# Optimization experiments

Measured on AMD Instinct MI355X. Metric: run time of the kernel, lower is better.

The kernel has to match this reference:

```python
import jax, jax.numpy as jnp
import numpy as np

TOKENS, DIM, DIM_OUT, R, ALPHA = 8192, 4096, 4096, 16, 32
SCALE = ALPHA / R  # 2.0


def setup_inputs() -> dict:
    key = jax.random.key(0)
    k1, k2, k3, k4, k5 = jax.random.split(key, 5)
    x = jax.random.normal(k1, (TOKENS, DIM), dtype=jnp.float32)
    A = jax.random.normal(k2, (DIM, R), dtype=jnp.float32)
    B = jax.random.normal(k3, (R, DIM_OUT), dtype=jnp.float32) * 0.02
    W = jax.random.normal(k4, (DIM_OUT, DIM), dtype=jnp.float32) * 0.02  # base Linear weight
    b = jax.random.normal(k5, (DIM_OUT,), dtype=jnp.float32)
    return {"x": x, "A": A, "B": B, "W": W, "b": b}


def reference(x, A, B, W, b):
    # LoRA path: x @ (A @ B) * scale, computed in the efficient low-rank order
    # (mathematically identical to materializing the full-rank weight).
    lora = ((x @ A) @ B) * SCALE              # [tokens, dim_out]
    base = x @ W.T + b                         # wrapped base Linear forward
    return lora + base
```

## Files before the change

### kernel.cpp

```cpp
#include <hip/hip_runtime.h>
#include <hip/hip_bf16.h>
#include <stdint.h>

#define TOKENS   8192
#define DIM      4096
#define DIM_OUT  4096
#define LORA_R   16
#define LORA_SCALE 2.0f

typedef __bf16 bf16_t;
typedef __attribute__((ext_vector_type(8))) __bf16 bfrag;
typedef __attribute__((ext_vector_type(4))) float f32x4;

__device__ __forceinline__ void gload_lds16(const bf16_t* gsrc, bf16_t* ldst) {
    __builtin_amdgcn_global_load_lds(
        (const __attribute__((address_space(1))) uint32_t*)(const void*)gsrc,
        (__attribute__((address_space(3))) uint32_t*)(void*)ldst,
        16, 0, 0);
}

__global__ void cast_x_kernel(const float* __restrict__ x, bf16_t* __restrict__ xb) {
    const int total = TOKENS * DIM / 8;
    for (int i = blockIdx.x * blockDim.x + threadIdx.x; i < total;
         i += gridDim.x * blockDim.x) {
        const float4* p = reinterpret_cast<const float4*>(x + (size_t)i * 8);
        float4 v0 = p[0], v1 = p[1];
        union { bf16_t o[8]; uint4 u; } pk;
        pk.o[0] = (bf16_t)v0.x; pk.o[1] = (bf16_t)v0.y;
        pk.o[2] = (bf16_t)v0.z; pk.o[3] = (bf16_t)v0.w;
        pk.o[4] = (bf16_t)v1.x; pk.o[5] = (bf16_t)v1.y;
        pk.o[6] = (bf16_t)v1.z; pk.o[7] = (bf16_t)v1.w;
        *reinterpret_cast<uint4*>(xb + (size_t)i * 8) = pk.u;
    }
}

__global__ void weff_kernel(const float* __restrict__ W, const float* __restrict__ A,
                            const float* __restrict__ B, bf16_t* __restrict__ Wt) {
    int idx = blockIdx.x * blockDim.x + threadIdx.x;
    int k0 = (idx & 511) << 3;
    int n0 = (idx >> 9) << 2;

    float bn[4][16];
#pragma unroll
    for (int r = 0; r < 16; ++r) {
        float4 bv = *reinterpret_cast<const float4*>(B + (size_t)r * DIM_OUT + n0);
        bn[0][r] = bv.x; bn[1][r] = bv.y; bn[2][r] = bv.z; bn[3][r] = bv.w;
    }
    float ab[4][8];
#pragma unroll
    for (int j = 0; j < 8; ++j) {
        const float4* ap = reinterpret_cast<const float4*>(A + (size_t)(k0 + j) * LORA_R);
        float4 a0 = ap[0], a1 = ap[1], a2 = ap[2], a3 = ap[3];
        float av[16] = {a0.x,a0.y,a0.z,a0.w,a1.x,a1.y,a1.z,a1.w,
                        a2.x,a2.y,a2.z,a2.w,a3.x,a3.y,a3.z,a3.w};
#pragma unroll
        for (int n = 0; n < 4; ++n) {
            float s = 0.f;
#pragma unroll
            for (int r = 0; r < 16; ++r) s += av[r] * bn[n][r];
            ab[n][j] = s;
        }
    }
#pragma unroll
    for (int n = 0; n < 4; ++n) {
        const float4* wp = reinterpret_cast<const float4*>(W + (size_t)(n0 + n) * DIM + k0);
        float4 w0 = wp[0], w1 = wp[1];
        float wv[8] = {w0.x,w0.y,w0.z,w0.w,w1.x,w1.y,w1.z,w1.w};
        union { bf16_t o[8]; uint4 u; } pk;
#pragma unroll
        for (int j = 0; j < 8; ++j) pk.o[j] = (bf16_t)(wv[j] + LORA_SCALE * ab[n][j]);
        *reinterpret_cast<uint4*>(Wt + (size_t)(n0 + n) * DIM + k0) = pk.u;
    }
}

#define BM 256
#define BN 256
#define BK 64
#define MB_BLKS (TOKENS / BM)
#define NB_BLKS (DIM_OUT / BN)
#define NT      (DIM / BK)

#define SB0() __builtin_amdgcn_sched_barrier(0)
#define BAR() do { SB0(); __builtin_amdgcn_s_barrier(); SB0(); } while (0)
#define LGKM0() do { asm volatile("s_waitcnt lgkmcnt(0)" ::: "memory"); SB0(); } while (0)
#define VMWAIT_(n) asm volatile("s_waitcnt vmcnt(" #n ")" ::: "memory")
#define VMWAIT(n) VMWAIT_(n)

__global__ __launch_bounds__(512, 2) void gemm_kernel(
    const bf16_t* __restrict__ Xb, const bf16_t* __restrict__ Wt,
    const float* __restrict__ bias, float* __restrict__ C)
{
    __shared__ __align__(16) bf16_t sA[2][BM][BK];
    __shared__ __align__(16) bf16_t sB[2][BN][BK];

    const int nwg = MB_BLKS * NB_BLKS;
    int bid = blockIdx.x;
    int swz = (bid & 7) * (nwg >> 3) + (bid >> 3);
    int bm = swz / NB_BLKS;
    int bn = swz % NB_BLKS;

    const int tid  = threadIdx.x;
    const int lane = tid & 63;
    const int wid  = tid >> 6;
    const int wr   = wid >> 2;
    const int wc   = wid & 3;

    const int srow = tid >> 3;
    const int scol = (tid & 7) * 8;
    const int koff = (((tid & 7) ^ ((tid >> 3) & 7)) * 8);
    const bf16_t* Ag = Xb + (size_t)(bm * BM + srow) * DIM + koff;
    const bf16_t* Bg = Wt + (size_t)(bn * BN + srow) * DIM + koff;

#define STAGE_A_H(dd, kt, h) do { \
    const bf16_t* s_ = Ag + (size_t)(kt) * BK + (size_t)((h) * 128) * DIM; \
    bf16_t* d_ = &sA[dd][(h) * 128 + srow][scol]; \
    gload_lds16(s_,                    d_); \
    gload_lds16(s_ + (size_t)64 * DIM, d_ + 64 * BK); \
} while (0)

#define STAGE_B_H(dd, kt, h) do { \
    const bf16_t* s_ = Bg + (size_t)(kt) * BK + (size_t)((h) * 128) * DIM; \
    bf16_t* d_ = &sB[dd][(h) * 128 + srow][scol]; \
    gload_lds16(s_,                    d_); \
    gload_lds16(s_ + (size_t)64 * DIM, d_ + 64 * BK); \
} while (0)

    const int q     = lane & 7;
    const int kslot = lane >> 4;
    const int r15   = lane & 15;
    const int cK0   = ((kslot    ) ^ q) * 8;
    const int cK1   = ((kslot + 4) ^ q) * 8;
    const int arow0 = wr * 128 + r15;
    const int brow0 = wc * 64  + r15;

    f32x4 acc[8][4] = {};
    bfrag a[4][2], bLo[2][2], bHi[2][2];

#define READ_A4(dst, dd, mb) do { \
    _Pragma("unroll") \
    for (int m_ = 0; m_ < 4; ++m_) { \
        dst[m_][0] = *reinterpret_cast<const bfrag*>(&sA[dd][arow0 + (mb + m_) * 16][cK0]); \
        dst[m_][1] = *reinterpret_cast<const bfrag*>(&sA[dd][arow0 + (mb + m_) * 16][cK1]); \
    } \
} while (0)

#define READ_B2(dst, dd, nb) do { \
    _Pragma("unroll") \
    for (int n_ = 0; n_ < 2; ++n_) { \
        dst[n_][0] = *reinterpret_cast<const bfrag*>(&sB[dd][brow0 + (nb + n_) * 16][cK0]); \
        dst[n_][1] = *reinterpret_cast<const bfrag*>(&sB[dd][brow0 + (nb + n_) * 16][cK1]); \
    } \
} while (0)

#define MFMA_Q(Af, Bf, mb, nb) do { \
    __builtin_amdgcn_s_setprio(1); \
    _Pragma("unroll") \
    for (int m_ = 0; m_ < 4; ++m_) \
    _Pragma("unroll") \
    for (int n_ = 0; n_ < 2; ++n_) \
    _Pragma("unroll") \
    for (int ks_ = 0; ks_ < 2; ++ks_) \
        acc[mb + m_][nb + n_] = __builtin_amdgcn_mfma_f32_16x16x32_bf16( \
            Af[m_][ks_], Bf[n_][ks_], acc[mb + m_][nb + n_], 0, 0, 0); \
    __builtin_amdgcn_s_setprio(0); \
} while (0)

#define TILE(d, kt, S1, S2, VM) do { \
     READ_A4(a, d, 0); READ_B2(bLo, d, 0); \
             BAR(); LGKM0(); MFMA_Q(a, bLo, 0, 0); BAR(); \
     READ_B2(bHi, d, 2); \
             if (S1) STAGE_A_H((d) ^ 1, (kt) + 1, 1); \
             BAR(); LGKM0(); MFMA_Q(a, bHi, 0, 2); BAR(); \
     READ_A4(a, d, 4); \
             if (S2) STAGE_B_H(d, (kt) + 2, 0); \
             BAR(); LGKM0(); MFMA_Q(a, bHi, 4, 2); BAR(); \
     if (S2) { STAGE_B_H(d, (kt) + 2, 1); STAGE_A_H(d, (kt) + 2, 0); } \
             BAR(); MFMA_Q(a, bLo, 4, 0); VMWAIT(VM); BAR(); \
} while (0)

    STAGE_A_H(0, 0, 0); STAGE_A_H(0, 0, 1); STAGE_B_H(0, 0, 0); STAGE_B_H(0, 0, 1);
    STAGE_A_H(1, 1, 0); STAGE_B_H(1, 1, 0); STAGE_B_H(1, 1, 1);
    VMWAIT(6);
    BAR();

    for (int it = 0; it < NT / 2 - 1; ++it) {
        int kt0 = 2 * it;
        TILE(0, kt0,     true, true, 6);
        TILE(1, kt0 + 1, true, true, 6);
    }
    TILE(0, 62, true,  false, 0);
    TILE(1, 63, false, false, 0);

    int row0 = bm * BM + wr * 128 + (lane >> 4) * 4;
    int col0 = bn * BN + wc * 64 + r15;
#pragma unroll
    for (int n = 0; n < 4; ++n) {
        int c = col0 + n * 16;
        float bv = bias[c];
#pragma unroll
        for (int m = 0; m < 8; ++m) {
            int r = row0 + m * 16;
#pragma unroll
            for (int j = 0; j < 4; ++j)
                C[(size_t)(r + j) * DIM_OUT + c] = acc[m][n][j] + bv;
        }
    }
}

extern "C" void kernel_launch(void* const* d_in, const int* in_sizes, int n_in,
                              void* d_out, int out_size, void* d_ws, size_t ws_size,
                              hipStream_t stream) {
    const float* x = (const float*)d_in[0];
    const float* A = (const float*)d_in[1];
    const float* B = (const float*)d_in[2];
    const float* W = (const float*)d_in[3];
    const float* b = (const float*)d_in[4];
    float* out = (float*)d_out;

    bf16_t* xb = (bf16_t*)d_ws;
    bf16_t* Wt = (bf16_t*)((char*)d_ws + (size_t)TOKENS * DIM * 2);

    cast_x_kernel<<<2048, 256, 0, stream>>>(x, xb);
    weff_kernel<<<(DIM_OUT * DIM / 32) / 256, 256, 0, stream>>>(W, A, B, Wt);
    gemm_kernel<<<MB_BLKS * NB_BLKS, 512, 0, stream>>>(xb, Wt, b, out);
}
```

Measured before the change: 346.4 us.

## Merge prep kernels, retile XCD block mapping, restructure GEMM staging pipeline

```diff
diff --git a/kernel.cpp b/kernel.cpp
--- a/kernel.cpp
+++ b/kernel.cpp
@@ -19,57 +19,59 @@
         16, 0, 0);
 }
 
-__global__ void cast_x_kernel(const float* __restrict__ x, bf16_t* __restrict__ xb) {
-    const int total = TOKENS * DIM / 8;
-    for (int i = blockIdx.x * blockDim.x + threadIdx.x; i < total;
-         i += gridDim.x * blockDim.x) {
-        const float4* p = reinterpret_cast<const float4*>(x + (size_t)i * 8);
-        float4 v0 = p[0], v1 = p[1];
-        union { bf16_t o[8]; uint4 u; } pk;
-        pk.o[0] = (bf16_t)v0.x; pk.o[1] = (bf16_t)v0.y;
-        pk.o[2] = (bf16_t)v0.z; pk.o[3] = (bf16_t)v0.w;
-        pk.o[4] = (bf16_t)v1.x; pk.o[5] = (bf16_t)v1.y;
-        pk.o[6] = (bf16_t)v1.z; pk.o[7] = (bf16_t)v1.w;
-        *reinterpret_cast<uint4*>(xb + (size_t)i * 8) = pk.u;
-    }
-}
-
-__global__ void weff_kernel(const float* __restrict__ W, const float* __restrict__ A,
+#define CAST_BLOCKS 2048
+__global__ void prep_kernel(const float* __restrict__ x, bf16_t* __restrict__ xb,
+                            const float* __restrict__ W, const float* __restrict__ A,
                             const float* __restrict__ B, bf16_t* __restrict__ Wt) {
-    int idx = blockIdx.x * blockDim.x + threadIdx.x;
-    int k0 = (idx & 511) << 3;
-    int n0 = (idx >> 9) << 2;
-
-    float bn[4][16];
-#pragma unroll
-    for (int r = 0; r < 16; ++r) {
-        float4 bv = *reinterpret_cast<const float4*>(B + (size_t)r * DIM_OUT + n0);
-        bn[0][r] = bv.x; bn[1][r] = bv.y; bn[2][r] = bv.z; bn[3][r] = bv.w;
-    }
-    float ab[4][8];
-#pragma unroll
-    for (int j = 0; j < 8; ++j) {
-        const float4* ap = reinterpret_cast<const float4*>(A + (size_t)(k0 + j) * LORA_R);
-        float4 a0 = ap[0], a1 = ap[1], a2 = ap[2], a3 = ap[3];
-        float av[16] = {a0.x,a0.y,a0.z,a0.w,a1.x,a1.y,a1.z,a1.w,
-                        a2.x,a2.y,a2.z,a2.w,a3.x,a3.y,a3.z,a3.w};
+    if (blockIdx.x < CAST_BLOCKS) {
+        const int total = TOKENS * DIM / 8;
+        for (int i = blockIdx.x * blockDim.x + threadIdx.x; i < total;
+             i += CAST_BLOCKS * 256) {
+            const float4* p = reinterpret_cast<const float4*>(x + (size_t)i * 8);
+            float4 v0 = p[0], v1 = p[1];
+            union { bf16_t o[8]; uint4 u; } pk;
+            pk.o[0] = (bf16_t)v0.x; pk.o[1] = (bf16_t)v0.y;
+            pk.o[2] = (bf16_t)v0.z; pk.o[3] = (bf16_t)v0.w;
+            pk.o[4] = (bf16_t)v1.x; pk.o[5] = (bf16_t)v1.y;
+            pk.o[6] = (bf16_t)v1.z; pk.o[7] = (bf16_t)v1.w;
+            *reinterpret_cast<uint4*>(xb + (size_t)i * 8) = pk.u;
+        }
+    } else {
+        int idx = (blockIdx.x - CAST_BLOCKS) * blockDim.x + threadIdx.x;
+        int k0 = (idx & 511) << 3;
+        int n0 = (idx >> 9) << 2;
+
+        float bn[4][16];
+#pragma unroll
+        for (int r = 0; r < 16; ++r) {
+            float4 bv = *reinterpret_cast<const float4*>(B + (size_t)r * DIM_OUT + n0);
+            bn[0][r] = bv.x; bn[1][r] = bv.y; bn[2][r] = bv.z; bn[3][r] = bv.w;
+        }
+        float ab[4][8];
+#pragma unroll
+        for (int j = 0; j < 8; ++j) {
+            const float4* ap = reinterpret_cast<const float4*>(A + (size_t)(k0 + j) * LORA_R);
+            float4 a0 = ap[0], a1 = ap[1], a2 = ap[2], a3 = ap[3];
+            float av[16] = {a0.x,a0.y,a0.z,a0.w,a1.x,a1.y,a1.z,a1.w,
+                            a2.x,a2.y,a2.z,a2.w,a3.x,a3.y,a3.z,a3.w};
+#pragma unroll
+            for (int n = 0; n < 4; ++n) {
+                float s = 0.f;
+#pragma unroll
+                for (int r = 0; r < 16; ++r) s += av[r] * bn[n][r];
+                ab[n][j] = s;
+            }
+        }
 #pragma unroll
         for (int n = 0; n < 4; ++n) {
-            float s = 0.f;
-#pragma unroll
-            for (int r = 0; r < 16; ++r) s += av[r] * bn[n][r];
-            ab[n][j] = s;
-        }
-    }
-#pragma unroll
-    for (int n = 0; n < 4; ++n) {
-        const float4* wp = reinterpret_cast<const float4*>(W + (size_t)(n0 + n) * DIM + k0);
-        float4 w0 = wp[0], w1 = wp[1];
-        float wv[8] = {w0.x,w0.y,w0.z,w0.w,w1.x,w1.y,w1.z,w1.w};
-        union { bf16_t o[8]; uint4 u; } pk;
-#pragma unroll
-        for (int j = 0; j < 8; ++j) pk.o[j] = (bf16_t)(wv[j] + LORA_SCALE * ab[n][j]);
-        *reinterpret_cast<uint4*>(Wt + (size_t)(n0 + n) * DIM + k0) = pk.u;
+            const float4* wp = reinterpret_cast<const float4*>(W + (size_t)(n0 + n) * DIM + k0);
+            float4 w0 = wp[0], w1 = wp[1];
+            float wv[8] = {w0.x,w0.y,w0.z,w0.w,w1.x,w1.y,w1.z,w1.w};
+            union { bf16_t o[8]; uint4 u; } pk;
+#pragma unroll
+            for (int j = 0; j < 8; ++j) pk.o[j] = (bf16_t)(wv[j] + LORA_SCALE * ab[n][j]);
+            *reinterpret_cast<uint4*>(Wt + (size_t)(n0 + n) * DIM + k0) = pk.u;
+        }
     }
 }
 
@@ -81,8 +83,6 @@
 #define NT      (DIM / BK)
 
 #define SB0() __builtin_amdgcn_sched_barrier(0)
-#define BAR() do { SB0(); __builtin_amdgcn_s_barrier(); SB0(); } while (0)
-#define LGKM0() do { asm volatile("s_waitcnt lgkmcnt(0)" ::: "memory"); SB0(); } while (0)
 #define VMWAIT_(n) asm volatile("s_waitcnt vmcnt(" #n ")" ::: "memory")
 #define VMWAIT(n) VMWAIT_(n)
 
@@ -93,11 +93,13 @@
     __shared__ __align__(16) bf16_t sA[2][BM][BK];
     __shared__ __align__(16) bf16_t sB[2][BN][BK];
 
-    const int nwg = MB_BLKS * NB_BLKS;
     int bid = blockIdx.x;
-    int swz = (bid & 7) * (nwg >> 3) + (bid >> 3);
-    int bm = swz / NB_BLKS;
-    int bn = swz % NB_BLKS;
+    int xcd = bid & 7;
+    int j   = bid >> 3;
+    int qq  = j >> 5;
+    int rr  = j & 31;
+    int bm  = xcd * 4 + (rr >> 3);
+    int bn  = (rr & 7) + 8 * qq;
 
     const int tid  = threadIdx.x;
     const int lane = tid & 63;
@@ -136,11 +138,11 @@
     f32x4 acc[8][4] = {};
     bfrag a[4][2], bLo[2][2], bHi[2][2];
 
-#define READ_A4(dst, dd, mb) do { \
+#define READ_A4(dd, mb) do { \
     _Pragma("unroll") \
     for (int m_ = 0; m_ < 4; ++m_) { \
-        dst[m_][0] = *reinterpret_cast<const bfrag*>(&sA[dd][arow0 + (mb + m_) * 16][cK0]); \
-        dst[m_][1] = *reinterpret_cast<const bfrag*>(&sA[dd][arow0 + (mb + m_) * 16][cK1]); \
+        a[m_][0] = *reinterpret_cast<const bfrag*>(&sA[dd][arow0 + (mb + m_) * 16][cK0]); \
+        a[m_][1] = *reinterpret_cast<const bfrag*>(&sA[dd][arow0 + (mb + m_) * 16][cK1]); \
     } \
 } while (0)
 
@@ -152,7 +154,13 @@
     } \
 } while (0)
 
-#define MFMA_Q(Af, Bf, mb, nb) do { \
+#define PSYNC() do { \
+    __builtin_amdgcn_s_barrier(); \
+    asm volatile("s_waitcnt lgkmcnt(0)" ::: "memory"); \
+    SB0(); \
+} while (0)
+
+#define MFMA_Q(Bf, mb, nb) do { \
     __builtin_amdgcn_s_setprio(1); \
     _Pragma("unroll") \
     for (int m_ = 0; m_ < 4; ++m_) \
@@ -161,35 +169,75 @@
     _Pragma("unroll") \
     for (int ks_ = 0; ks_ < 2; ++ks_) \
         acc[mb + m_][nb + n_] = __builtin_amdgcn_mfma_f32_16x16x32_bf16( \
-            Af[m_][ks_], Bf[n_][ks_], acc[mb + m_][nb + n_], 0, 0, 0); \
+            a[m_][ks_], Bf[n_][ks_], acc[mb + m_][nb + n_], 0, 0, 0); \
     __builtin_amdgcn_s_setprio(0); \
 } while (0)
 
-#define TILE(d, kt, S1, S2, VM) do { \
-     READ_A4(a, d, 0); READ_B2(bLo, d, 0); \
-             BAR(); LGKM0(); MFMA_Q(a, bLo, 0, 0); BAR(); \
-     READ_B2(bHi, d, 2); \
-             if (S1) STAGE_A_H((d) ^ 1, (kt) + 1, 1); \
-             BAR(); LGKM0(); MFMA_Q(a, bHi, 0, 2); BAR(); \
-     READ_A4(a, d, 4); \
-             if (S2) STAGE_B_H(d, (kt) + 2, 0); \
-             BAR(); LGKM0(); MFMA_Q(a, bHi, 4, 2); BAR(); \
-     if (S2) { STAGE_B_H(d, (kt) + 2, 1); STAGE_A_H(d, (kt) + 2, 0); } \
-             BAR(); MFMA_Q(a, bLo, 4, 0); VMWAIT(VM); BAR(); \
-} while (0)
-
-    STAGE_A_H(0, 0, 0); STAGE_A_H(0, 0, 1); STAGE_B_H(0, 0, 0); STAGE_B_H(0, 0, 1);
-    STAGE_A_H(1, 1, 0); STAGE_B_H(1, 1, 0); STAGE_B_H(1, 1, 1);
-    VMWAIT(6);
-    BAR();
+#define EBAR() __builtin_amdgcn_s_barrier()
+
+#define TILEPAIR(u, S, VMn) do { \
+     READ_A4(0, 0); READ_B2(bLo, 0, 0); STAGE_A_H(1, (u) + 1, 0); \
+             PSYNC(); MFMA_Q(bLo, 0, 0); EBAR(); \
+     READ_B2(bHi, 0, 2); STAGE_A_H(1, (u) + 1, 1); \
+             PSYNC(); MFMA_Q(bHi, 0, 2); EBAR(); \
+     READ_A4(0, 4); if (S) STAGE_B_H(0, (u) + 2, 0); \
+             PSYNC(); MFMA_Q(bHi, 4, 2); EBAR(); \
+     if (S) STAGE_B_H(0, (u) + 2, 1); \
+             __builtin_amdgcn_s_barrier(); \
+             MFMA_Q(bLo, 4, 0); VMWAIT(VMn); EBAR(); \
+     READ_A4(1, 0); READ_B2(bLo, 1, 0); if (S) STAGE_A_H(0, (u) + 2, 0); \
+             PSYNC(); MFMA_Q(bLo, 0, 0); EBAR(); \
+     READ_B2(bHi, 1, 2); if (S) STAGE_A_H(0, (u) + 2, 1); \
+             PSYNC(); MFMA_Q(bHi, 0, 2); EBAR(); \
+     READ_A4(1, 4); if (S) STAGE_B_H(1, (u) + 3, 0); \
+             PSYNC(); MFMA_Q(bHi, 4, 2); EBAR(); \
+     if (S) STAGE_B_H(1, (u) + 3, 1); \
+             __builtin_amdgcn_s_barrier(); \
+             MFMA_Q(bLo, 4, 0); VMWAIT(0); EBAR(); \
+} while (0)
+
+    STAGE_A_H(0, 0, 0); STAGE_A_H(0, 0, 1);
+    STAGE_B_H(0, 0, 0); STAGE_B_H(0, 0, 1);
+    STAGE_B_H(1, 1, 0); STAGE_B_H(1, 1, 1);
+    VMWAIT(4);
+    EBAR();
 
     for (int it = 0; it < NT / 2 - 1; ++it) {
-        int kt0 = 2 * it;
-        TILE(0, kt0,     true, true, 6);
-        TILE(1, kt0 + 1, true, true, 6);
+        int u = 2 * it;
+         READ_A4(0, 0); READ_B2(bLo, 0, 0); STAGE_A_H(1, u + 1, 0);
+                 PSYNC(); MFMA_Q(bLo, 0, 0); EBAR();
+         READ_B2(bHi, 0, 2); STAGE_A_H(1, u + 1, 1);
+                 PSYNC(); MFMA_Q(bHi, 0, 2); EBAR();
+         READ_A4(0, 4); STAGE_B_H(0, u + 2, 0);
+                 PSYNC(); MFMA_Q(bHi, 4, 2); EBAR();
+         STAGE_B_H(0, u + 2, 1);
+                 __builtin_amdgcn_s_barrier();
+                 MFMA_Q(bLo, 4, 0); VMWAIT(4); EBAR();
+         READ_A4(1, 0); READ_B2(bLo, 1, 0); STAGE_A_H(0, u + 2, 0);
+                 PSYNC(); MFMA_Q(bLo, 0, 0); EBAR();
+         READ_B2(bHi, 1, 2); STAGE_A_H(0, u + 2, 1);
+                 PSYNC(); MFMA_Q(bHi, 0, 2); EBAR();
+         READ_A4(1, 4); STAGE_B_H(1, u + 3, 0);
+                 PSYNC(); MFMA_Q(bHi, 4, 2); EBAR();
+         STAGE_B_H(1, u + 3, 1);
+                 __builtin_amdgcn_s_barrier();
+                 MFMA_Q(bLo, 4, 0); VMWAIT(4); EBAR();
     }
-    TILE(0, 62, true,  false, 0);
-    TILE(1, 63, false, false, 0);
+     READ_A4(0, 0); READ_B2(bLo, 0, 0); STAGE_A_H(1, 63, 0);
+             PSYNC(); MFMA_Q(bLo, 0, 0); EBAR();
+     READ_B2(bHi, 0, 2); STAGE_A_H(1, 63, 1);
+             PSYNC(); MFMA_Q(bHi, 0, 2); EBAR();
+     READ_A4(0, 4);
+             PSYNC(); MFMA_Q(bHi, 4, 2); EBAR();
+     __builtin_amdgcn_s_barrier();
+             MFMA_Q(bLo, 4, 0); VMWAIT(0); EBAR();
+     READ_A4(1, 0); READ_B2(bLo, 1, 0);
+             PSYNC(); MFMA_Q(bLo, 0, 0); EBAR();
+     READ_B2(bHi, 1, 2);
+             PSYNC(); MFMA_Q(bHi, 0, 2); EBAR();
+     READ_A4(1, 4);
+             PSYNC(); MFMA_Q(bHi, 4, 2); EBAR();
+     MFMA_Q(bLo, 4, 0);
 
     int row0 = bm * BM + wr * 128 + (lane >> 4) * 4;
     int col0 = bn * BN + wc * 64 + r15;
@@ -201,8 +249,8 @@
         for (int m = 0; m < 8; ++m) {
             int r = row0 + m * 16;
 #pragma unroll
-            for (int j = 0; j < 4; ++j)
-                C[(size_t)(r + j) * DIM_OUT + c] = acc[m][n][j] + bv;
+            for (int jj = 0; jj < 4; ++jj)
+                C[(size_t)(r + jj) * DIM_OUT + c] = acc[m][n][jj] + bv;
         }
     }
 }
@@ -220,7 +268,6 @@
     bf16_t* xb = (bf16_t*)d_ws;
     bf16_t* Wt = (bf16_t*)((char*)d_ws + (size_t)TOKENS * DIM * 2);
 
-    cast_x_kernel<<<2048, 256, 0, stream>>>(x, xb);
-    weff_kernel<<<(DIM_OUT * DIM / 32) / 256, 256, 0, stream>>>(W, A, B, Wt);
+    prep_kernel<<<CAST_BLOCKS + 2048, 256, 0, stream>>>(x, xb, W, A, B, Wt);
     gemm_kernel<<<MB_BLKS * NB_BLKS, 512, 0, stream>>>(xb, Wt, b, out);
 }
```

Measured after the change: 327.5 us. 5.5% less time.
